# Kernel optimization log

Hardware: AMD Instinct MI355X
Metric: run time of the kernel (lower is better)

## Reference

```python
import jax, jax.numpy as jnp
import numpy as np

# Module hyperparameters (init_kwargs)
N_CLASSES = 21
RADIUS = 5
SIZE = (256, 256)
SIGMA_DIST = 4.0
SIGMA_FEAT = 1.0
B, C = 8, 32


def _offsets(radius):
    """Integer (dy, dx) offsets with Euclidean distance < radius (includes (0,0))."""
    offs = []
    r = int(radius)
    for dy in range(-r + 1, r):
        for dx in range(-r + 1, r):
            if dy * dy + dx * dx < radius * radius:
                offs.append((dy, dx))
    return offs


OFFSETS = _offsets(RADIUS)  # 69 offsets for radius=5


def setup_inputs() -> dict:
    key = jax.random.key(0)
    k1, k2 = jax.random.split(key)
    H, W = SIZE
    classification = jax.random.uniform(k1, (B, N_CLASSES, H, W), dtype=jnp.float32)
    features = jax.random.normal(k2, (B, C, H, W), dtype=jnp.float32)
    return {"classification": classification, "features": features}


def reference(classification, features):
    # classification: [B, K, H, W] soft assignments S
    # features:       [B, C, H, W]
    Bb, K, H, W = classification.shape
    inv_sd2 = 1.0 / (SIGMA_DIST * SIGMA_DIST)
    inv_sf2 = 1.0 / (SIGMA_FEAT * SIGMA_FEAT)

    hs = jnp.arange(H)
    ws = jnp.arange(W)

    WS = jnp.zeros_like(classification)           # (W @ S), [B, K, H, W]
    degree = jnp.zeros((Bb, H, W), classification.dtype)

    # Loop over the small fixed set of neighbor offsets (69 for radius=5).
    for dy, dx in OFFSETS:
        f_nb = jnp.roll(features, (-dy, -dx), axis=(2, 3))
        s_nb = jnp.roll(classification, (-dy, -dx), axis=(2, 3))
        # mask out wrap-around: neighbor (h+dy, w+dx) must be in-bounds
        valid_h = (hs + dy >= 0) & (hs + dy < H)
        valid_w = (ws + dx >= 0) & (ws + dx < W)
        mask = (valid_h[:, None] & valid_w[None, :]).astype(classification.dtype)
        # Gaussian affinity: distance kernel * feature kernel
        feat_d2 = ((features - f_nb) ** 2).sum(axis=1)        # [B, H, W]
        w = jnp.exp(-(dy * dy + dx * dx) * inv_sd2 - feat_d2 * inv_sf2) * mask
        WS = WS + w[:, None] * s_nb
        degree = degree + w

    # numerator   = S^T W S : [B, K, K]
    # denominator = d^T S   : [B, K]
    num = jnp.einsum('bkhw,bjhw->bkj', classification, WS)
    den = jnp.einsum('bhw,bkhw->bk', degree, classification)
    return (num / den[:, None, :]).sum()
```

## Files before the change

### kernel.cpp

```cpp
#include <hip/hip_runtime.h>

#define HH 256
#define WW 256
#define HWPX 65536
#define BB 8
#define KK 21
#define CC 32
#define NT 8192
#define E_LOG2E 1.4426950408889634f
#define PEN -30000.0f

typedef _Float16 half2v __attribute__((ext_vector_type(2)));
typedef _Float16 half8  __attribute__((ext_vector_type(8)));
typedef float    f32x4v __attribute__((ext_vector_type(4)));
union F4H { float4 f4; half2v h[4]; half8 h8; };

__global__ __launch_bounds__(256) void prep(const float* __restrict__ cls,
                                            const float* __restrict__ feat,
                                            float4* __restrict__ fpk,
                                            float2* __restrict__ TN) {
    const int tid = blockIdx.x * 256 + threadIdx.x;
    const int b = tid >> 16;
    const int p = tid & (HWPX - 1);

    const float* cbase = cls + (size_t)b * KK * HWPX + p;
    float T = 0.f;
#pragma unroll
    for (int k = 0; k < KK; ++k) T += cbase[(size_t)k * HWPX];

    const float* src = feat + (size_t)b * CC * HWPX + p;
    float nq = 0.f;
#pragma unroll
    for (int j = 0; j < 4; ++j) {
        F4H u;
#pragma unroll
        for (int k = 0; k < 4; ++k) {
            float a  = src[(size_t)(j * 8 + 2 * k) * HWPX];
            float b2 = src[(size_t)(j * 8 + 2 * k + 1) * HWPX];
            u.h[k] = __builtin_bit_cast(half2v, __builtin_amdgcn_cvt_pkrtz(a, b2));
            nq = __builtin_amdgcn_fdot2(u.h[k], u.h[k], nq, false);
        }
        fpk[(size_t)j * (BB * HWPX) + tid] = u.f4;
    }
    TN[tid] = make_float2(T, nq);
}

__global__ __launch_bounds__(256) void affinity_mfma(const float4* __restrict__ fpk,
                                                     const float2* __restrict__ TN,
                                                     const float* __restrict__ cls,
                                                     float* __restrict__ partial) {
    __shared__ float smN[4][21], smD[4][21];
    const int L    = blockIdx.x;
    const int b    = L & 7;
    const int t    = L >> 3;
    const int wid  = threadIdx.x >> 6;
    const int lane = threadIdx.x & 63;
    const int g    = lane >> 4;
    const int c    = lane & 15;
    const int idx  = t * 4 + wid;
    const int y0   = (idx >> 5) * 2;
    const int x0   = (idx & 31) * 8;

    const size_t bofs = (size_t)b * HWPX;
    const float4* fb  = fpk + bofs;
    const float2* tnb = TN + bofs;

    F4H afr;
    afr.f4 = fb[(size_t)g * (BB * HWPX) + ((y0 + (c & 1)) << 8) + x0 + (c >> 1)];

    int pxr[4];
    float npE[4];
#pragma unroll
    for (int r = 0; r < 4; ++r) {
        pxr[r] = ((y0 + (r & 1)) << 8) + x0 + 2 * g + (r >> 1);
        npE[r] = tnb[pxr[r]].y * E_LOG2E;
    }

    const int xbu  = x0 - 4 + c;
    const bool inb = (unsigned)xbu < WW;
    const int xbc  = min(max(xbu, 0), WW - 1);
    const int voffF = (g * (BB * HWPX) + xbc) * 16;
    const int voffT = xbc * 8;

    float cst0[4], cst1[4], cst4[4], cst9[4], cst16[4];
#pragma unroll
    for (int r = 0; r < 4; ++r) {
        const int dx = c - 4 - 2 * g - (r >> 1);
        const int s2 = dx * dx;
        cst0[r]  = (inb && s2 <= 16) ? fmaf((float)(s2 + 0),  -E_LOG2E / 16.f, -npE[r]) : PEN;
        cst1[r]  = (inb && s2 <= 16) ? fmaf((float)(s2 + 1),  -E_LOG2E / 16.f, -npE[r]) : PEN;
        cst4[r]  = (inb && s2 <= 16) ? fmaf((float)(s2 + 4),  -E_LOG2E / 16.f, -npE[r]) : PEN;
        cst9[r]  = (inb && s2 <= 9)  ? fmaf((float)(s2 + 9),  -E_LOG2E / 16.f, -npE[r]) : PEN;
        cst16[r] = (inb && s2 <= 4)  ? fmaf((float)(s2 + 16), -E_LOG2E / 16.f, -npE[r]) : PEN;
    }

    const f32x4v czero = {0.f, 0.f, 0.f, 0.f};
    float pdeg[4] = {0.f, 0.f, 0.f, 0.f};
    float pV[4]   = {0.f, 0.f, 0.f, 0.f};

    const char* fpkB = (const char*)fpk + bofs * 16;
    const char* tnB  = (const char*)TN + bofs * 8;

    auto body = [&](int ny, const float (&ce)[4], const float (&co)[4], int mode) {
        if ((unsigned)ny >= HH) return;
        const char* pF = fpkB + ((size_t)ny << 12);
        const char* pT = tnB  + ((size_t)ny << 11);
        F4H bfr; bfr.f4 = *(const float4*)(pF + voffF);
        const float2 tq = *(const float2*)(pT + voffT);
        f32x4v cz = __builtin_amdgcn_mfma_f32_16x16x32_f16(afr.h8, bfr.h8, czero, 0, 0, 0);
        const float t1 = tq.y * -E_LOG2E;
        if (mode != 2) {
            const float e0 = fmaf(cz[0], 2.f * E_LOG2E, ce[0] + t1);
            const float w0 = __builtin_exp2f(e0);
            pdeg[0] += w0;  pV[0] = fmaf(w0, tq.x, pV[0]);
            const float e2 = fmaf(cz[2], 2.f * E_LOG2E, ce[2] + t1);
            const float w2 = __builtin_exp2f(e2);
            pdeg[2] += w2;  pV[2] = fmaf(w2, tq.x, pV[2]);
        }
        if (mode != 1) {
            const float e1 = fmaf(cz[1], 2.f * E_LOG2E, co[1] + t1);
            const float w1 = __builtin_exp2f(e1);
            pdeg[1] += w1;  pV[1] = fmaf(w1, tq.x, pV[1]);
            const float e3 = fmaf(cz[3], 2.f * E_LOG2E, co[3] + t1);
            const float w3 = __builtin_exp2f(e3);
            pdeg[3] += w3;  pV[3] = fmaf(w3, tq.x, pV[3]);
        }
    };

    body(y0 - 4, cst16, cst16, 1);
    body(y0 - 3, cst9,  cst16, 0);
    body(y0 - 2, cst4,  cst9,  0);
    body(y0 - 1, cst1,  cst4,  0);
    body(y0 + 0, cst0,  cst1,  0);
    body(y0 + 1, cst1,  cst0,  0);
    body(y0 + 2, cst4,  cst1,  0);
    body(y0 + 3, cst9,  cst4,  0);
    body(y0 + 4, cst16, cst9,  0);
    body(y0 + 5, cst16, cst16, 2);

#pragma unroll
    for (int m = 1; m <= 8; m <<= 1) {
#pragma unroll
        for (int r = 0; r < 4; ++r) {
            pdeg[r] += __shfl_xor(pdeg[r], m, 64);
            pV[r]   += __shfl_xor(pV[r], m, 64);
        }
    }

    float n0 = 0.f, d0 = 0.f, n1 = 0.f, d1 = 0.f;
    const float* clsb = cls + (size_t)b * KK * HWPX;
#pragma unroll
    for (int r = 0; r < 4; ++r) {
        const float s0 = clsb[(size_t)c * HWPX + pxr[r]];
        n0 = fmaf(s0, pV[r], n0);
        d0 = fmaf(s0, pdeg[r], d0);
        if (c < 5) {
            const float s1 = clsb[(size_t)(c + 16) * HWPX + pxr[r]];
            n1 = fmaf(s1, pV[r], n1);
            d1 = fmaf(s1, pdeg[r], d1);
        }
    }
#pragma unroll
    for (int m = 16; m <= 32; m <<= 1) {
        n0 += __shfl_xor(n0, m, 64);
        d0 += __shfl_xor(d0, m, 64);
        n1 += __shfl_xor(n1, m, 64);
        d1 += __shfl_xor(d1, m, 64);
    }
    if (lane < 16) {
        smN[wid][lane] = n0;
        smD[wid][lane] = d0;
        if (lane < 5) { smN[wid][16 + lane] = n1; smD[wid][16 + lane] = d1; }
    }
    __syncthreads();
    if (threadIdx.x < 2 * KK) {
        const int jq = threadIdx.x;
        const float v = (jq < KK)
            ? (smN[0][jq] + smN[1][jq] + smN[2][jq] + smN[3][jq])
            : (smD[0][jq - KK] + smD[1][jq - KK] + smD[2][jq - KK] + smD[3][jq - KK]);
        partial[(size_t)jq * NT + (size_t)b * 1024 + t] = v;
    }
}

__global__ __launch_bounds__(256) void reduce_part(const float* __restrict__ partial,
                                                   float* __restrict__ numer,
                                                   float* __restrict__ denom) {
    __shared__ float sm[4];
    const int jq = blockIdx.x;
    const int b  = blockIdx.y;
    const float* src = partial + (size_t)jq * NT + (size_t)b * 1024;
    float a = src[threadIdx.x] + src[threadIdx.x + 256]
            + src[threadIdx.x + 512] + src[threadIdx.x + 768];
#pragma unroll
    for (int off = 32; off > 0; off >>= 1) a += __shfl_down(a, off);
    if ((threadIdx.x & 63) == 0) sm[threadIdx.x >> 6] = a;
    __syncthreads();
    if (threadIdx.x == 0) {
        const float v = sm[0] + sm[1] + sm[2] + sm[3];
        if (jq < KK) numer[b * KK + jq] = v;
        else         denom[b * KK + jq - KK] = v;
    }
}

__global__ __launch_bounds__(256) void finalize(const float* __restrict__ numer,
                                                const float* __restrict__ denom,
                                                float* __restrict__ out) {
    __shared__ float sm[4];
    int i = threadIdx.x;
    float r = 0.f;
    if (i < BB * KK) r = numer[i] / denom[i];
#pragma unroll
    for (int off = 32; off > 0; off >>= 1) r += __shfl_down(r, off);
    if ((i & 63) == 0) sm[i >> 6] = r;
    __syncthreads();
    if (i == 0) out[0] = sm[0] + sm[1] + sm[2] + sm[3];
}

extern "C" void kernel_launch(void* const* d_in, const int* in_sizes, int n_in,
                              void* d_out, int out_size, void* d_ws, size_t ws_size,
                              hipStream_t stream) {
    const float* cls  = (const float*)d_in[0];
    const float* feat = (const float*)d_in[1];
    float* out = (float*)d_out;

    const size_t BHW = (size_t)BB * HWPX;
    float4* fpk     = (float4*)d_ws;
    float2* TN      = (float2*)((char*)d_ws + BHW * 64);
    float*  partial = (float*)((char*)TN + BHW * 8);
    float*  numer   = partial + (size_t)2 * KK * NT;
    float*  denom   = numer + BB * KK;

    prep<<<dim3((BB * HWPX) / 256), dim3(256), 0, stream>>>(cls, feat, fpk, TN);
    affinity_mfma<<<dim3(NT), dim3(256), 0, stream>>>(fpk, TN, cls, partial);
    reduce_part<<<dim3(2 * KK, BB), dim3(256), 0, stream>>>(partial, numer, denom);
    finalize<<<dim3(1), dim3(256), 0, stream>>>(numer, denom, out);
}
```

Before: 179.0 us.

## Prefetch all neighbor rows before MFMA loop and fuse final reductions

In the affinity kernel, the ten neighbor-row fragment and T/norm loads are now issued up front into register arrays, using clamped row indices, and the MFMA/exp work runs afterwards. This is meant to hide load latency, at the cost of extra registers; a launch_bounds occupancy hint is added to cap register use. The separate reduce and finalize kernels are merged into one that reduces numerator and denominator per (class, batch) and atomically adds the ratio into the output, which prep zeroes. This removes one launch but makes the floating-point summation order nondeterministic.

```diff
diff --git a/kernel.cpp b/kernel.cpp
--- a/kernel.cpp
+++ b/kernel.cpp
@@ -18,8 +18,10 @@
 __global__ __launch_bounds__(256) void prep(const float* __restrict__ cls,
                                             const float* __restrict__ feat,
                                             float4* __restrict__ fpk,
-                                            float2* __restrict__ TN) {
+                                            float2* __restrict__ TN,
+                                            float* __restrict__ out) {
     const int tid = blockIdx.x * 256 + threadIdx.x;
+    if (tid == 0) out[0] = 0.f;
     const int b = tid >> 16;
     const int p = tid & (HWPX - 1);
 
@@ -45,10 +47,10 @@
     TN[tid] = make_float2(T, nq);
 }
 
-__global__ __launch_bounds__(256) void affinity_mfma(const float4* __restrict__ fpk,
-                                                     const float2* __restrict__ TN,
-                                                     const float* __restrict__ cls,
-                                                     float* __restrict__ partial) {
+__global__ __launch_bounds__(256, 4) void affinity_mfma(const float4* __restrict__ fpk,
+                                                        const float2* __restrict__ TN,
+                                                        const float* __restrict__ cls,
+                                                        float* __restrict__ partial) {
     __shared__ float smN[4][21], smD[4][21];
     const int L    = blockIdx.x;
     const int b    = L & 7;
@@ -94,49 +96,56 @@
         cst16[r] = (inb && s2 <= 4)  ? fmaf((float)(s2 + 16), -E_LOG2E / 16.f, -npE[r]) : PEN;
     }
 
+    const char* fpkB = (const char*)fpk + bofs * 16;
+    const char* tnB  = (const char*)TN + bofs * 8;
+
+    F4H   bfr[10];
+    float2 tqv[10];
+#pragma unroll
+    for (int i = 0; i < 10; ++i) {
+        const int nyr = min(max(y0 - 4 + i, 0), HH - 1);
+        bfr[i].f4 = *(const float4*)(fpkB + ((size_t)nyr << 12) + voffF);
+        tqv[i]    = *(const float2*)(tnB  + ((size_t)nyr << 11) + voffT);
+    }
+
     const f32x4v czero = {0.f, 0.f, 0.f, 0.f};
     float pdeg[4] = {0.f, 0.f, 0.f, 0.f};
     float pV[4]   = {0.f, 0.f, 0.f, 0.f};
 
-    const char* fpkB = (const char*)fpk + bofs * 16;
-    const char* tnB  = (const char*)TN + bofs * 8;
-
-    auto body = [&](int ny, const float (&ce)[4], const float (&co)[4], int mode) {
-        if ((unsigned)ny >= HH) return;
-        const char* pF = fpkB + ((size_t)ny << 12);
-        const char* pT = tnB  + ((size_t)ny << 11);
-        F4H bfr; bfr.f4 = *(const float4*)(pF + voffF);
-        const float2 tq = *(const float2*)(pT + voffT);
-        f32x4v cz = __builtin_amdgcn_mfma_f32_16x16x32_f16(afr.h8, bfr.h8, czero, 0, 0, 0);
-        const float t1 = tq.y * -E_LOG2E;
-        if (mode != 2) {
-            const float e0 = fmaf(cz[0], 2.f * E_LOG2E, ce[0] + t1);
-            const float w0 = __builtin_exp2f(e0);
-            pdeg[0] += w0;  pV[0] = fmaf(w0, tq.x, pV[0]);
-            const float e2 = fmaf(cz[2], 2.f * E_LOG2E, ce[2] + t1);
-            const float w2 = __builtin_exp2f(e2);
-            pdeg[2] += w2;  pV[2] = fmaf(w2, tq.x, pV[2]);
-        }
-        if (mode != 1) {
-            const float e1 = fmaf(cz[1], 2.f * E_LOG2E, co[1] + t1);
-            const float w1 = __builtin_exp2f(e1);
-            pdeg[1] += w1;  pV[1] = fmaf(w1, tq.x, pV[1]);
-            const float e3 = fmaf(cz[3], 2.f * E_LOG2E, co[3] + t1);
-            const float w3 = __builtin_exp2f(e3);
-            pdeg[3] += w3;  pV[3] = fmaf(w3, tq.x, pV[3]);
-        }
-    };
-
-    body(y0 - 4, cst16, cst16, 1);
-    body(y0 - 3, cst9,  cst16, 0);
-    body(y0 - 2, cst4,  cst9,  0);
-    body(y0 - 1, cst1,  cst4,  0);
-    body(y0 + 0, cst0,  cst1,  0);
-    body(y0 + 1, cst1,  cst0,  0);
-    body(y0 + 2, cst4,  cst1,  0);
-    body(y0 + 3, cst9,  cst4,  0);
-    body(y0 + 4, cst16, cst9,  0);
-    body(y0 + 5, cst16, cst16, 2);
+#define BODY(I, CE, CO, MODE)                                                            \
+    if ((unsigned)(y0 - 4 + (I)) < HH) {                                                 \
+        f32x4v cz = __builtin_amdgcn_mfma_f32_16x16x32_f16(afr.h8, bfr[I].h8, czero, 0, 0, 0); \
+        const float t1 = tqv[I].y * -E_LOG2E;                                            \
+        const float tx = tqv[I].x;                                                       \
+        if ((MODE) != 2) {                                                               \
+            const float e0 = fmaf(cz[0], 2.f * E_LOG2E, (CE)[0] + t1);                   \
+            const float w0 = __builtin_exp2f(e0);                                        \
+            pdeg[0] += w0;  pV[0] = fmaf(w0, tx, pV[0]);                                 \
+            const float e2 = fmaf(cz[2], 2.f * E_LOG2E, (CE)[2] + t1);                   \
+            const float w2 = __builtin_exp2f(e2);                                        \
+            pdeg[2] += w2;  pV[2] = fmaf(w2, tx, pV[2]);                                 \
+        }                                                                                \
+        if ((MODE) != 1) {                                                               \
+            const float e1 = fmaf(cz[1], 2.f * E_LOG2E, (CO)[1] + t1);                   \
+            const float w1 = __builtin_exp2f(e1);                                        \
+            pdeg[1] += w1;  pV[1] = fmaf(w1, tx, pV[1]);                                 \
+            const float e3 = fmaf(cz[3], 2.f * E_LOG2E, (CO)[3] + t1);                   \
+            const float w3 = __builtin_exp2f(e3);                                        \
+            pdeg[3] += w3;  pV[3] = fmaf(w3, tx, pV[3]);                                 \
+        }                                                                                \
+    }
+
+    BODY(0, cst16, cst16, 1)
+    BODY(1, cst9,  cst16, 0)
+    BODY(2, cst4,  cst9,  0)
+    BODY(3, cst1,  cst4,  0)
+    BODY(4, cst0,  cst1,  0)
+    BODY(5, cst1,  cst0,  0)
+    BODY(6, cst4,  cst1,  0)
+    BODY(7, cst9,  cst4,  0)
+    BODY(8, cst16, cst9,  0)
+    BODY(9, cst16, cst16, 2)
+#undef BODY
 
 #pragma unroll
     for (int m = 1; m <= 8; m <<= 1) {
@@ -182,38 +191,27 @@
     }
 }
 
-__global__ __launch_bounds__(256) void reduce_part(const float* __restrict__ partial,
-                                                   float* __restrict__ numer,
-                                                   float* __restrict__ denom) {
-    __shared__ float sm[4];
-    const int jq = blockIdx.x;
-    const int b  = blockIdx.y;
-    const float* src = partial + (size_t)jq * NT + (size_t)b * 1024;
-    float a = src[threadIdx.x] + src[threadIdx.x + 256]
-            + src[threadIdx.x + 512] + src[threadIdx.x + 768];
-#pragma unroll
-    for (int off = 32; off > 0; off >>= 1) a += __shfl_down(a, off);
-    if ((threadIdx.x & 63) == 0) sm[threadIdx.x >> 6] = a;
+__global__ __launch_bounds__(256) void reduce_fin(const float* __restrict__ partial,
+                                                  float* __restrict__ out) {
+    __shared__ float smn[4], smd[4];
+    const int j = blockIdx.x;
+    const int b = blockIdx.y;
+    const float4 n4 = ((const float4*)(partial + (size_t)j        * NT + (size_t)b * 1024))[threadIdx.x];
+    const float4 d4 = ((const float4*)(partial + (size_t)(j + KK) * NT + (size_t)b * 1024))[threadIdx.x];
+    float n = (n4.x + n4.y) + (n4.z + n4.w);
+    float d = (d4.x + d4.y) + (d4.z + d4.w);
+#pragma unroll
+    for (int off = 32; off > 0; off >>= 1) {
+        n += __shfl_down(n, off);
+        d += __shfl_down(d, off);
+    }
+    if ((threadIdx.x & 63) == 0) { smn[threadIdx.x >> 6] = n; smd[threadIdx.x >> 6] = d; }
     __syncthreads();
     if (threadIdx.x == 0) {
-        const float v = sm[0] + sm[1] + sm[2] + sm[3];
-        if (jq < KK) numer[b * KK + jq] = v;
-        else         denom[b * KK + jq - KK] = v;
-    }
-}
-
-__global__ __launch_bounds__(256) void finalize(const float* __restrict__ numer,
-                                                const float* __restrict__ denom,
-                                                float* __restrict__ out) {
-    __shared__ float sm[4];
-    int i = threadIdx.x;
-    float r = 0.f;
-    if (i < BB * KK) r = numer[i] / denom[i];
-#pragma unroll
-    for (int off = 32; off > 0; off >>= 1) r += __shfl_down(r, off);
-    if ((i & 63) == 0) sm[i >> 6] = r;
-    __syncthreads();
-    if (i == 0) out[0] = sm[0] + sm[1] + sm[2] + sm[3];
+        const float N = (smn[0] + smn[1]) + (smn[2] + smn[3]);
+        const float D = (smd[0] + smd[1]) + (smd[2] + smd[3]);
+        atomicAdd(out, N / D);
+    }
 }
 
 extern "C" void kernel_launch(void* const* d_in, const int* in_sizes, int n_in,
@@ -227,11 +225,8 @@
     float4* fpk     = (float4*)d_ws;
     float2* TN      = (float2*)((char*)d_ws + BHW * 64);
     float*  partial = (float*)((char*)TN + BHW * 8);
-    float*  numer   = partial + (size_t)2 * KK * NT;
-    float*  denom   = numer + BB * KK;
-
-    prep<<<dim3((BB * HWPX) / 256), dim3(256), 0, stream>>>(cls, feat, fpk, TN);
+
+    prep<<<dim3((BB * HWPX) / 256), dim3(256), 0, stream>>>(cls, feat, fpk, TN, out);
     affinity_mfma<<<dim3(NT), dim3(256), 0, stream>>>(fpk, TN, cls, partial);
-    reduce_part<<<dim3(2 * KK, BB), dim3(256), 0, stream>>>(partial, numer, denom);
-    finalize<<<dim3(1), dim3(256), 0, stream>>>(numer, denom, out);
-}
+    reduce_fin<<<dim3(KK, BB), dim3(256), 0, stream>>>(partial, out);
+}
```

New measurement: 184.6 us. 1.03x slower.
